# Kernel optimization log

Measured on AMD Instinct MI355X. Metric: run time of the kernel, lower is better.

## Reference

```python
import jax, jax.numpy as jnp
import numpy as np

PACK = 8  # 32 bits / 4 bits per value


def _unpack_int4(packed):
    # packed: [..., O//8] int32 -> [..., O] int32 nibbles in [0, 16)
    shifts = jnp.arange(PACK, dtype=jnp.int32) * 4
    nib = (packed[..., None] >> shifts) & jnp.int32(0xF)
    return nib.reshape(*packed.shape[:-1], packed.shape[-1] * PACK)


def setup_inputs() -> dict:
    key = jax.random.key(0)
    k1, k2, k3, k4 = jax.random.split(key, 4)
    I, O, GS = 4096, 11008, 128
    G = I // GS
    x = jax.random.normal(k1, (4096, I), dtype=jnp.float32)
    qweight = jax.random.randint(k2, (I, O // PACK), -2**31, 2**31 - 1, dtype=jnp.int32)
    scales = jax.random.uniform(k3, (G, O), dtype=jnp.float32) * 0.01 + 1e-3
    qzeros = jax.random.randint(k4, (G, O // PACK), -2**31, 2**31 - 1, dtype=jnp.int32)
    return {"x": x, "qweight": qweight, "scales": scales, "qzeros": qzeros, "group_size": GS}


def reference(x, qweight, scales, qzeros, group_size):
    I = qweight.shape[0]
    O = qweight.shape[1] * PACK
    G = I // group_size
    w_int = _unpack_int4(qweight)                       # [I, O] int32
    z_int = _unpack_int4(qzeros)                        # [G, O] int32
    # dequant: (w - zero_of_group) * scale_of_group
    w_grp = w_int.reshape(G, group_size, O).astype(jnp.float32)
    w_deq = (w_grp - z_int[:, None, :].astype(jnp.float32)) * scales[:, None, :]
    w_deq = w_deq.reshape(I, O)                         # [I, O] float32
    return x @ w_deq                                    # [N, O]
```

## Files before the change

kernel.cpp:

```cpp
#include <hip/hip_runtime.h>
#include <hip/hip_bf16.h>
#include <stdint.h>

#define M_DIM 4096
#define K_DIM 4096
#define N_DIM 11008
#define OPACK (N_DIM / 8)
#define GSZ   128

#define NIT 32

typedef __attribute__((ext_vector_type(8))) short short8;
typedef __attribute__((ext_vector_type(4))) float floatx4;
typedef __attribute__((ext_vector_type(4))) unsigned int uintx4;

static __device__ __forceinline__ unsigned short f32_to_bf16_rne(float f) {
    union { float f; unsigned int u; } c; c.f = f;
    unsigned int u = c.u;
    u += 0x7fffu + ((u >> 16) & 1u);
    return (unsigned short)(u >> 16);
}

static __device__ __forceinline__ void load16_lds(const void* gptr, void* lptr) {
    __builtin_amdgcn_global_load_lds(
        (__attribute__((address_space(1))) void*)gptr,
        (__attribute__((address_space(3))) void*)lptr,
        16, 0, 0);
}

__global__ __launch_bounds__(256)
void convert_x_kernel(const float* __restrict__ x, unsigned short* __restrict__ xb) {
    const int idx = (blockIdx.x * 256 + threadIdx.x) * 8;
    floatx4 v0 = *(const floatx4*)(x + idx);
    floatx4 v1 = *(const floatx4*)(x + idx + 4);
    unsigned short r[8];
#pragma unroll
    for (int i = 0; i < 4; i++) {
        r[i]     = f32_to_bf16_rne(v0[i]);
        r[4 + i] = f32_to_bf16_rne(v1[i]);
    }
    *(uintx4*)(xb + idx) = *(const uintx4*)r;
}

__global__ __launch_bounds__(256)
void dequant_kernel(const int* __restrict__ qweight, const float* __restrict__ scales,
                    const int* __restrict__ qzeros, unsigned short* __restrict__ Wt) {
    const int o  = blockIdx.x * 256 + threadIdx.x;
    const int i0 = blockIdx.y * 64;
    const int g  = i0 >> 7;
    const int op = o >> 3;
    const int sh = (o & 7) * 4;
    const int z  = (qzeros[g * OPACK + op] >> sh) & 15;
    const float s = scales[g * N_DIM + o];
    unsigned short buf[64];
#pragma unroll
    for (int k = 0; k < 64; k++) {
        const int q   = qweight[(i0 + k) * OPACK + op];
        const float w = (float)(((q >> sh) & 15) - z) * s;
        buf[k] = f32_to_bf16_rne(w);
    }
    uintx4* dst = (uintx4*)(Wt + (size_t)o * K_DIM + i0);
    const uintx4* src = (const uintx4*)buf;
#pragma unroll
    for (int t = 0; t < 8; t++) dst[t] = src[t];
}


#define STAGE_A(KB, RG) do {                                   \
    const char* g_ = ApS + (size_t)(KB) * 64;                  \
    char* l_ = (char*)lds_a[RG] + tid * 16;                    \
    load16_lds(g_, l_);                                        \
    load16_lds(g_ + (1u << 20), l_ + 8192);                    \
} while (0)

#define STAGE_B(KB, RG) do {                                   \
    const char* g_ = BpS + (size_t)(KB) * 64;                  \
    char* l_ = (char*)lds_b[RG] + tid * 16;                    \
    load16_lds(g_, l_);                                        \
    load16_lds(g_ + (1u << 20), l_ + 8192);                    \
} while (0)

#define VM4 asm volatile("s_waitcnt vmcnt(4)" ::: "memory")
#define VM0 asm volatile("s_waitcnt vmcnt(0)" ::: "memory")
#define VM_NONE ((void)0)

#define LDA_FRAGS(RG_, RH_) do {                                                  \
    const short* Ar_ = &lds_a[RG_][a_off + (RH_) * 2048];                         \
    _Pragma("unroll")                                                             \
    for (int f_ = 0; f_ < 4; ++f_) av[f_] = *(const short8*)(Ar_ + f_ * 512);     \
} while (0)

#define LDB_FRAGS(RG_) do {                                                       \
    const short* Br_ = &lds_b[RG_][b_off];                                        \
    _Pragma("unroll")                                                             \
    for (int n_ = 0; n_ < 4; ++n_) bv[n_] = *(const short8*)(Br_ + n_ * 512);     \
} while (0)

#define PHASE(H_, RG_, RH_, LB_, RDC_, VMW_, STG_) do {                              \
    __builtin_amdgcn_s_setprio(1);                                                   \
    _Pragma("unroll")                                                                \
    for (int f_ = 0; f_ < 4; ++f_)                                                   \
        _Pragma("unroll")                                                            \
        for (int n_ = 0; n_ < 4; ++n_)                                               \
            acc[(H_) * 4 + f_][n_] = __builtin_amdgcn_mfma_f32_16x16x32_bf16(        \
                av[f_], bv[n_], acc[(H_) * 4 + f_][n_], 0, 0, 0);                    \
    __builtin_amdgcn_s_setprio(0);                                                   \
    __builtin_amdgcn_sched_barrier(0);                                               \
    VMW_;                                                                            \
    if (RDC_) { LDA_FRAGS(RG_, RH_); if (LB_) LDB_FRAGS(RG_); }                      \
    STG_;                                                                            \
    asm volatile("s_barrier" ::: "memory");                                          \
} while (0)

__global__ __launch_bounds__(512, 2)
void gemm_kernel(const unsigned short* __restrict__ X,
                 const unsigned short* __restrict__ Wt,
                 float* __restrict__ C) {
    __shared__ __align__(16) short lds_a[4][8192];
    __shared__ __align__(16) short lds_b[4][8192];

    const int tid  = threadIdx.x;
    const int wave = tid >> 6;
    const int lane = tid & 63;
    const int wm   = wave >> 2;
    const int wn   = wave & 3;

    const int pid    = blockIdx.x;
    const int L      = (pid & 7) * 86 + (pid >> 3);
    const int m_tile = L & 15;
    const int n_tile = L >> 4;
    const int m0 = m_tile * 256;
    const int n0 = n_tile * 256;

    const int row_l = tid >> 2;
    const int cl    = (tid & 3) ^ ((tid >> 3) & 3);
    const char* ApS = (const char*)X  + ((size_t)(m0 + row_l) << 13) + (cl << 4);
    const char* BpS = (const char*)Wt + ((size_t)(n0 + row_l) << 13) + (cl << 4);

    const int l15 = lane & 15;
    const int kcs = (lane >> 4) ^ ((lane >> 1) & 3);
    const int a_off = (wm * 128 + l15) * 32 + kcs * 8;
    const int b_off = (wn * 64  + l15) * 32 + kcs * 8;

    floatx4 acc[8][4] = {};
    short8 av[4], bv[4];

    STAGE_B(0, 0); STAGE_A(0, 0);
    STAGE_B(1, 1); STAGE_A(1, 1);
    STAGE_B(2, 2); STAGE_A(2, 2);
    STAGE_B(3, 3);
    asm volatile("s_waitcnt vmcnt(6)" ::: "memory");
    asm volatile("s_barrier" ::: "memory");
    LDA_FRAGS(0, 0);
    LDB_FRAGS(0);

#pragma unroll 1
    for (int i = 0; i < NIT; ++i) {
        const int  kb4  = 4 * i;
        const bool more = (i + 1 < NIT);
        PHASE(0, 0, 1, 0, 1, VM_NONE,                  STAGE_A(kb4 + 3, 3));
        PHASE(1, 1, 0, 1, 1, VM4,                      if (more) STAGE_B(kb4 + 4, 0));
        PHASE(0, 1, 1, 0, 1, VM_NONE,                  if (more) STAGE_A(kb4 + 4, 0));
        PHASE(1, 2, 0, 1, 1, if (more) VM4; else VM0,  if (more) STAGE_B(kb4 + 5, 1));
        PHASE(0, 2, 1, 0, 1, VM_NONE,                  if (more) STAGE_A(kb4 + 5, 1));
        PHASE(1, 3, 0, 1, 1, if (more) VM4,            if (more) STAGE_B(kb4 + 6, 2));
        PHASE(0, 3, 1, 0, 1, VM_NONE,                  if (more) STAGE_A(kb4 + 6, 2));
        PHASE(1, 0, 0, 1, more, if (more) VM4,         if (more) STAGE_B(kb4 + 7, 3));
    }

    const int crow = (lane >> 4) * 4;
#pragma unroll
    for (int f = 0; f < 8; ++f) {
#pragma unroll
        for (int n = 0; n < 4; ++n) {
            float* Cp = C + (size_t)(m0 + wm * 128 + f * 16 + crow) * N_DIM
                          + (n0 + wn * 64 + n * 16 + l15);
#pragma unroll
            for (int r = 0; r < 4; ++r)
                __builtin_nontemporal_store(acc[f][n][r], Cp + (size_t)r * N_DIM);
        }
    }
}

extern "C" void kernel_launch(void* const* d_in, const int* in_sizes, int n_in,
                              void* d_out, int out_size, void* d_ws, size_t ws_size,
                              hipStream_t stream) {
    const float* x       = (const float*)d_in[0];
    const int*   qweight = (const int*)d_in[1];
    const float* scales  = (const float*)d_in[2];
    const int*   qzeros  = (const int*)d_in[3];
    float* out = (float*)d_out;

    unsigned short* Xb = (unsigned short*)d_ws;
    unsigned short* Wt = (unsigned short*)((char*)d_ws + (size_t)M_DIM * K_DIM * 2);

    convert_x_kernel<<<(M_DIM * K_DIM) / (256 * 8), 256, 0, stream>>>(x, Xb);
    dequant_kernel<<<dim3(N_DIM / 256, K_DIM / 64), 256, 0, stream>>>(qweight, scales, qzeros, Wt);
    gemm_kernel<<<(M_DIM / 256) * (N_DIM / 256), 512, 0, stream>>>(Xb, Wt, out);
}
```

Before: 616.1 us.

## Double-buffer MFMA register fragments and transpose dequant output through LDS

The GEMM main loop now keeps two register sets for the A and B fragments. The next phase's LDS reads are issued before the current phase's MFMAs, so LDS latency overlaps with compute; the waitcnt schedule and the sched_barrier are adjusted to match. Separately, the dequant kernel stages its bf16 output through a swizzled LDS tile so that global writes to the transposed weight are coalesced across threads instead of one row per thread. The extra fragment registers raise register pressure under the 2-blocks-per-SM launch bound, and the retuned vmcnt waits must stay correct.

```diff
diff --git a/kernel.cpp b/kernel.cpp
--- a/kernel.cpp
+++ b/kernel.cpp
@@ -45,13 +45,18 @@
 __global__ __launch_bounds__(256)
 void dequant_kernel(const int* __restrict__ qweight, const float* __restrict__ scales,
                     const int* __restrict__ qzeros, unsigned short* __restrict__ Wt) {
-    const int o  = blockIdx.x * 256 + threadIdx.x;
-    const int i0 = blockIdx.y * 64;
-    const int g  = i0 >> 7;
-    const int op = o >> 3;
-    const int sh = (o & 7) * 4;
-    const int z  = (qzeros[g * OPACK + op] >> sh) & 15;
+    __shared__ __align__(16) unsigned short tile[256][64];
+
+    const int tid = threadIdx.x;
+    const int o0  = blockIdx.x * 256;
+    const int i0  = blockIdx.y * 64;
+    const int o   = o0 + tid;
+    const int g   = i0 >> 7;
+    const int op  = o >> 3;
+    const int sh  = (o & 7) * 4;
+    const int z   = (qzeros[g * OPACK + op] >> sh) & 15;
     const float s = scales[g * N_DIM + o];
+
     unsigned short buf[64];
 #pragma unroll
     for (int k = 0; k < 64; k++) {
@@ -59,10 +64,19 @@
         const float w = (float)(((q >> sh) & 15) - z) * s;
         buf[k] = f32_to_bf16_rne(w);
     }
-    uintx4* dst = (uintx4*)(Wt + (size_t)o * K_DIM + i0);
-    const uintx4* src = (const uintx4*)buf;
-#pragma unroll
-    for (int t = 0; t < 8; t++) dst[t] = src[t];
+#pragma unroll
+    for (int c = 0; c < 8; c++)
+        *(uintx4*)&tile[tid][(c ^ (tid & 7)) * 8] = *(const uintx4*)&buf[c * 8];
+
+    __syncthreads();
+
+    const int c_out = tid & 7;
+#pragma unroll
+    for (int j = 0; j < 8; j++) {
+        const int r = (tid >> 3) + j * 32;
+        const uintx4 v = *(const uintx4*)&tile[r][(c_out ^ (r & 7)) * 8];
+        *(uintx4*)&Wt[(size_t)(o0 + r) * K_DIM + i0 + c_out * 8] = v;
+    }
 }
 
 
@@ -80,35 +94,34 @@
     load16_lds(g_ + (1u << 20), l_ + 8192);                    \
 } while (0)
 
+#define VM8 asm volatile("s_waitcnt vmcnt(8)" ::: "memory")
 #define VM4 asm volatile("s_waitcnt vmcnt(4)" ::: "memory")
 #define VM0 asm volatile("s_waitcnt vmcnt(0)" ::: "memory")
 #define VM_NONE ((void)0)
 
-#define LDA_FRAGS(RG_, RH_) do {                                                  \
-    const short* Ar_ = &lds_a[RG_][a_off + (RH_) * 2048];                         \
-    _Pragma("unroll")                                                             \
-    for (int f_ = 0; f_ < 4; ++f_) av[f_] = *(const short8*)(Ar_ + f_ * 512);     \
-} while (0)
-
-#define LDB_FRAGS(RG_) do {                                                       \
-    const short* Br_ = &lds_b[RG_][b_off];                                        \
-    _Pragma("unroll")                                                             \
-    for (int n_ = 0; n_ < 4; ++n_) bv[n_] = *(const short8*)(Br_ + n_ * 512);     \
-} while (0)
-
-#define PHASE(H_, RG_, RH_, LB_, RDC_, VMW_, STG_) do {                              \
+#define PHASE(H_, MAV_, MBV_, RAV_, RBV_, ARG_, AH_, DOB_, BRG_, RDC_, VMW_, STG_) do { \
+    if (RDC_) {                                                                      \
+        const short* Ar_ = &lds_a[ARG_][a_off + (AH_) * 2048];                       \
+        _Pragma("unroll")                                                            \
+        for (int f_ = 0; f_ < 4; ++f_)                                               \
+            av[RAV_][f_] = *(const short8*)(Ar_ + f_ * 512);                         \
+        if (DOB_) {                                                                  \
+            const short* Br_ = &lds_b[BRG_][b_off];                                  \
+            _Pragma("unroll")                                                        \
+            for (int n_ = 0; n_ < 4; ++n_)                                           \
+                bv[RBV_][n_] = *(const short8*)(Br_ + n_ * 512);                     \
+        }                                                                            \
+    }                                                                                \
+    STG_;                                                                            \
     __builtin_amdgcn_s_setprio(1);                                                   \
     _Pragma("unroll")                                                                \
     for (int f_ = 0; f_ < 4; ++f_)                                                   \
         _Pragma("unroll")                                                            \
         for (int n_ = 0; n_ < 4; ++n_)                                               \
             acc[(H_) * 4 + f_][n_] = __builtin_amdgcn_mfma_f32_16x16x32_bf16(        \
-                av[f_], bv[n_], acc[(H_) * 4 + f_][n_], 0, 0, 0);                    \
+                av[MAV_][f_], bv[MBV_][n_], acc[(H_) * 4 + f_][n_], 0, 0, 0);        \
     __builtin_amdgcn_s_setprio(0);                                                   \
-    __builtin_amdgcn_sched_barrier(0);                                               \
     VMW_;                                                                            \
-    if (RDC_) { LDA_FRAGS(RG_, RH_); if (LB_) LDB_FRAGS(RG_); }                      \
-    STG_;                                                                            \
     asm volatile("s_barrier" ::: "memory");                                          \
 } while (0)
 
@@ -143,29 +156,35 @@
     const int b_off = (wn * 64  + l15) * 32 + kcs * 8;
 
     floatx4 acc[8][4] = {};
-    short8 av[4], bv[4];
+    short8 av[2][4], bv[2][4];
 
     STAGE_B(0, 0); STAGE_A(0, 0);
     STAGE_B(1, 1); STAGE_A(1, 1);
     STAGE_B(2, 2); STAGE_A(2, 2);
     STAGE_B(3, 3);
-    asm volatile("s_waitcnt vmcnt(6)" ::: "memory");
+    asm volatile("s_waitcnt vmcnt(10)" ::: "memory");
     asm volatile("s_barrier" ::: "memory");
-    LDA_FRAGS(0, 0);
-    LDB_FRAGS(0);
+    {
+        const short* Ar = &lds_a[0][a_off];
+        const short* Br = &lds_b[0][b_off];
+#pragma unroll
+        for (int f = 0; f < 4; ++f) av[0][f] = *(const short8*)(Ar + f * 512);
+#pragma unroll
+        for (int n = 0; n < 4; ++n) bv[0][n] = *(const short8*)(Br + n * 512);
+    }
 
 #pragma unroll 1
     for (int i = 0; i < NIT; ++i) {
         const int  kb4  = 4 * i;
         const bool more = (i + 1 < NIT);
-        PHASE(0, 0, 1, 0, 1, VM_NONE,                  STAGE_A(kb4 + 3, 3));
-        PHASE(1, 1, 0, 1, 1, VM4,                      if (more) STAGE_B(kb4 + 4, 0));
-        PHASE(0, 1, 1, 0, 1, VM_NONE,                  if (more) STAGE_A(kb4 + 4, 0));
-        PHASE(1, 2, 0, 1, 1, if (more) VM4; else VM0,  if (more) STAGE_B(kb4 + 5, 1));
-        PHASE(0, 2, 1, 0, 1, VM_NONE,                  if (more) STAGE_A(kb4 + 5, 1));
-        PHASE(1, 3, 0, 1, 1, if (more) VM4,            if (more) STAGE_B(kb4 + 6, 2));
-        PHASE(0, 3, 1, 0, 1, VM_NONE,                  if (more) STAGE_A(kb4 + 6, 2));
-        PHASE(1, 0, 0, 1, more, if (more) VM4,         if (more) STAGE_B(kb4 + 7, 3));
+        PHASE(0, 0, 0, 1, 0, 0, 1, 0, 0, 1,    VM8,                      STAGE_A(kb4 + 3, 3));
+        PHASE(1, 1, 0, 0, 1, 1, 0, 1, 1, 1,    VM_NONE,                  if (more) STAGE_B(kb4 + 4, 0));
+        PHASE(0, 0, 1, 1, 0, 1, 1, 0, 0, 1,    if (more) VM8; else VM4,  if (more) STAGE_A(kb4 + 4, 0));
+        PHASE(1, 1, 1, 0, 0, 2, 0, 1, 2, 1,    VM_NONE,                  if (more) STAGE_B(kb4 + 5, 1));
+        PHASE(0, 0, 0, 1, 0, 2, 1, 0, 0, 1,    if (more) VM8; else VM0,  if (more) STAGE_A(kb4 + 5, 1));
+        PHASE(1, 1, 0, 0, 1, 3, 0, 1, 3, 1,    VM_NONE,                  if (more) STAGE_B(kb4 + 6, 2));
+        PHASE(0, 0, 1, 1, 0, 3, 1, 0, 0, 1,    if (more) VM8,            if (more) STAGE_A(kb4 + 6, 2));
+        PHASE(1, 1, 1, 0, 0, 0, 0, 1, 0, more, VM_NONE,                  if (more) STAGE_B(kb4 + 7, 3));
     }
 
     const int crow = (lane >> 4) * 4;
```

New measurement: 613.7 us. No clear change (-0.4%).
